# Kernel tuning notes

Hardware: AMD Instinct MI355X
Metric: run time of the kernel (lower is better)

Reference implementation:

```python
import jax, jax.numpy as jnp
import numpy as np

B, N, K = 4, 2048, 20
TD, GD = 64, 128          # trans_dim, graph_dim
OBJ, IMG = 200, 224       # obj_size, img_size
EPS = 1e-5
G = 4                     # GroupNorm groups


def setup_inputs() -> dict:
    key = jax.random.key(0)
    ks = jax.random.split(key, 16)
    nrm = lambda k, shp, s=0.05: jax.random.normal(k, shp, jnp.float32) * s
    inp = {}
    inp["original_pc"] = jax.random.uniform(ks[0], (B, N, 3), jnp.float32)
    inp["pc"] = jax.random.uniform(ks[1], (B, N, 3), jnp.float32)
    # input_trans: Conv1d(3, TD, 1)
    inp["W_in"] = nrm(ks[2], (TD, 3)); inp["b_in"] = jnp.zeros((TD,), jnp.float32)
    # graph_layer: Conv2d(2*TD, GD, 1, bias=False) + GroupNorm(4, GD)
    inp["W_graph"] = nrm(ks[3], (GD, 2 * TD))
    inp["gn_g"] = jnp.ones((GD,), jnp.float32); inp["gn_b"] = jnp.zeros((GD,), jnp.float32)
    # proj_layer: Conv1d(GD, GD, 1)
    inp["W_proj"] = nrm(ks[4], (GD, GD)); inp["b_proj"] = jnp.zeros((GD,), jnp.float32)
    # BasicBlock: conv3x3 + BN (eval) x2
    inp["W1"] = nrm(ks[5], (GD, GD, 3, 3))
    inp["bn1_g"] = jnp.ones((GD,), jnp.float32); inp["bn1_b"] = jnp.zeros((GD,), jnp.float32)
    inp["bn1_m"] = nrm(ks[6], (GD,), 0.1)
    inp["bn1_v"] = jax.random.uniform(ks[7], (GD,), jnp.float32, 0.5, 1.5)
    inp["W2"] = nrm(ks[8], (GD, GD, 3, 3))
    inp["bn2_g"] = jnp.ones((GD,), jnp.float32); inp["bn2_b"] = jnp.zeros((GD,), jnp.float32)
    inp["bn2_m"] = nrm(ks[9], (GD,), 0.1)
    inp["bn2_v"] = jax.random.uniform(ks[10], (GD,), jnp.float32, 0.5, 1.5)
    # img_block tail: Conv2d(GD, GD, 1)
    inp["W_imgc"] = nrm(ks[11], (GD, GD)); inp["b_imgc"] = jnp.zeros((GD,), jnp.float32)
    # img_layer: Conv2d(GD, 3, 1)
    inp["W_img"] = nrm(ks[12], (3, GD)); inp["b_img"] = jnp.zeros((3,), jnp.float32)
    return inp


def reference(original_pc, pc, W_in, b_in, W_graph, gn_g, gn_b, W_proj, b_proj,
              W1, bn1_g, bn1_b, bn1_m, bn1_v, W2, bn2_g, bn2_b, bn2_m, bn2_v,
              W_imgc, b_imgc, W_img, b_img):
    # ---- point feature + knn graph feature ----
    x = jnp.einsum('bnd,cd->bnc', original_pc, W_in) + b_in              # (B,N,TD)
    sq = jnp.sum(original_pc * original_pc, -1)                          # (B,N)
    d2 = sq[:, :, None] + sq[:, None, :] - 2.0 * jnp.einsum('bnd,bmd->bnm', original_pc, original_pc)
    _, idx = jax.lax.top_k(-d2, K)                                       # (B,N,K) knn indices
    nbr = jax.vmap(lambda a, i: a[i])(x, idx)                            # (B,N,K,TD) gather
    xq = x[:, :, None, :]
    feat = jnp.concatenate([nbr - xq, jnp.broadcast_to(xq, nbr.shape)], -1)  # (B,N,K,2TD)
    # edge-conv 1x1 + GroupNorm(4) + LeakyReLU(0.2)
    y = jnp.einsum('bnkc,oc->bnko', feat, W_graph)                       # (B,N,K,GD)
    yg = y.reshape(B, N, K, G, GD // G)
    mu = yg.mean(axis=(1, 2, 4), keepdims=True)
    var = yg.var(axis=(1, 2, 4), keepdims=True)
    y = ((yg - mu) / jnp.sqrt(var + EPS)).reshape(B, N, K, GD) * gn_g + gn_b
    y = jax.nn.leaky_relu(y, 0.2)
    f = y.max(axis=2)                                                    # (B,N,GD) max over k
    f = jnp.einsum('bnc,oc->bno', f, W_proj) + b_proj                    # (B,N,GD)

    # ---- dense-to-grid index math ----
    pmin = pc.min(axis=1); pmax = pc.max(axis=1)                         # (B,3)
    gs = jnp.max((pmax - pmin)[:, :2], axis=-1) / (OBJ - 3)              # (B,)
    ixy = jnp.floor((pc[:, :, :2] - pmin[:, None, :2]) / gs[:, None, None])
    off9 = jnp.array([[-1, -1], [-1, 0], [-1, 1], [0, -1], [0, 0], [0, 1],
                      [1, -1], [1, 0], [1, 1]], jnp.float32)
    dense = (ixy[:, :, None, :] + off9[None, None]).reshape(B, N * 9, 2) + 1.0
    center = jnp.floor((dense.max(axis=1) + dense.min(axis=1)) / 2.0)    # (B,2)
    shift = OBJ / 2 - center - 1.0
    dense = dense + shift[:, None, :]
    lin = (dense[..., 0] * OBJ + dense[..., 1]).astype(jnp.int32)        # (B, N*9)

    fd = jnp.broadcast_to(f[:, :, None, :], (B, N, 9, GD)).reshape(B, N * 9, GD)
    seg = lin + (jnp.arange(B, dtype=jnp.int32) * (OBJ * OBJ))[:, None]
    grid = jax.ops.segment_sum(fd.reshape(-1, GD), seg.reshape(-1), num_segments=B * OBJ * OBJ)
    grid = grid.reshape(B, OBJ, OBJ, GD)
    pad = (IMG - OBJ) // 2
    res = jnp.pad(grid, ((0, 0), (pad, pad), (pad, pad), (0, 0)))
    res = res.transpose(0, 3, 1, 2)                                      # (B,GD,IMG,IMG)

    # ---- BasicBlock (eval BN) + 1x1 convs ----
    conv3 = lambda a, w: jax.lax.conv_general_dilated(a, w, (1, 1), 'SAME',
                         dimension_numbers=('NCHW', 'OIHW', 'NCHW'))
    bn = lambda a, g, b, m, v: (a - m[:, None, None]) / jnp.sqrt(v[:, None, None] + EPS) * g[:, None, None] + b[:, None, None]
    h = jax.nn.relu(bn(conv3(res, W1), bn1_g, bn1_b, bn1_m, bn1_v))
    h = bn(conv3(h, W2), bn2_g, bn2_b, bn2_m, bn2_v)
    h = jax.nn.relu(h + res)
    h = jnp.einsum('bchw,oc->bohw', h, W_imgc) + b_imgc[:, None, None]
    img = jnp.einsum('bchw,oc->bohw', h, W_img) + b_img[:, None, None]
    img = jax.nn.sigmoid(img)
    mean = jnp.array([0.485, 0.456, 0.406], jnp.float32)[None, :, None, None]
    std = jnp.array([0.229, 0.224, 0.225], jnp.float32)[None, :, None, None]
    return (img - mean) / std
```

## Files before the change

### kernel.cpp

```cpp
#include <hip/hip_runtime.h>
#include <stdint.h>

#define NPTS 2048
#define BATCH 4
#define KNN 20
#define EPSV 1e-5f

typedef short bf16x8 __attribute__((ext_vector_type(8)));
typedef float f32x4 __attribute__((ext_vector_type(4)));

__device__ __forceinline__ unsigned short f2bf(float f){
  union { float f; uint32_t u; } x; x.f = f;
  uint32_t u = x.u;
  uint32_t r = (u + 0x7fffu + ((u >> 16) & 1u)) >> 16;
  return (unsigned short)r;
}
__device__ __forceinline__ float bf2f(unsigned short h){
  union { uint32_t u; float f; } x; x.u = ((uint32_t)h) << 16;
  return x.f;
}

__global__ __launch_bounds__(256) void fold_wpk(const float* __restrict__ W, const float* __restrict__ g,
    const float* __restrict__ bb, const float* __restrict__ m, const float* __restrict__ vv,
    unsigned short* __restrict__ w, float* __restrict__ bias){
  int e = blockIdx.x*256 + threadIdx.x;
  if (e < 128){
    float s = g[e] / sqrtf(vv[e] + EPSV);
    bias[e] = bb[e] - m[e]*s;
  }
  if (e < 9*128*128){
    int t = e >> 14;
    int o = (e >> 7) & 127;
    int i = e & 127;
    int kh = t/3, kw = t - 3*kh;
    float s = g[o] / sqrtf(vv[o] + EPSV);
    float wv = W[((o*128 + i)*3 + kh)*3 + kw] * s;
    w[(t*128 + o)*128 + i] = f2bf(wv);
  }
}

__global__ __launch_bounds__(256) void fold_img(const float* __restrict__ Wimgc, const float* __restrict__ bimgc,
    const float* __restrict__ Wimg, const float* __restrict__ bimg,
    float* __restrict__ Wf, float* __restrict__ bf){
  int e = blockIdx.x*256 + threadIdx.x;
  if (e < 384){
    int j = e >> 7, c = e & 127;
    float s = 0.f;
    for (int o = 0; o < 128; ++o) s += Wimg[j*128+o] * Wimgc[o*128+c];
    Wf[e] = s;
  }
  if (e < 3){
    float s = bimg[e];
    for (int o = 0; o < 128; ++o) s += Wimg[e*128+o] * bimgc[o];
    bf[e] = s;
  }
}

__global__ __launch_bounds__(256) void prep_x(const float* __restrict__ opc, const float* __restrict__ Win,
    const float* __restrict__ bin, float* __restrict__ x, double* __restrict__ sq){
  int p = blockIdx.x*256 + threadIdx.x;
  if (p >= BATCH*NPTS) return;
  float a = opc[p*3], b = opc[p*3+1], c = opc[p*3+2];
  double ad = a, bd = b, cd = c;
  sq[p] = (ad*ad + bd*bd) + cd*cd;
  for (int o = 0; o < 64; ++o)
    x[p*64+o] = a*Win[o*3] + b*Win[o*3+1] + c*Win[o*3+2] + bin[o];
}

__global__ __launch_bounds__(256) void prep_uv(const float* __restrict__ x, const float* __restrict__ Wg,
    float* __restrict__ u, float* __restrict__ v){
  int e = blockIdx.x*256 + threadIdx.x;
  if (e >= BATCH*NPTS*128) return;
  int p = e >> 7, o = e & 127;
  const float* xr = x + p*64;
  const float* w = Wg + o*128;
  float su = 0.f, sv = 0.f;
  for (int c = 0; c < 64; ++c){
    float xv = xr[c];
    sv += w[c]*xv;
    su += (w[64+c] - w[c])*xv;
  }
  u[e] = su; v[e] = sv;
}

__device__ __forceinline__ void knn_merge(double va, int ia, double vb, int ib,
                                          double& vo, int& io){
  if (vb < va || (vb == va && ib < ia)){ vo = vb; io = ib; }
  else { vo = va; io = ia; }
}

__device__ __forceinline__ void knn_scan_q(const double* __restrict__ d, int lane, int qt,
                                           double& vq, int& iq){
  double v0 = 1.0e300, v1 = 1.0e300;
  int i0 = -1, i1 = -1;
  int kb = qt*8;
  #pragma unroll
  for (int k2 = 0; k2 < 8; k2 += 2){
    int m0 = lane + (kb + k2)*64;
    int m1 = lane + (kb + k2 + 1)*64;
    double a0 = d[m0];
    double a1 = d[m1];
    if (a0 < v0){ v0 = a0; i0 = m0; }
    if (a1 < v1){ v1 = a1; i1 = m1; }
  }
  knn_merge(v0, i0, v1, i1, vq, iq);
}

__global__ __launch_bounds__(128) void knn_k(const float* __restrict__ pc, const double* __restrict__ sq,
    int* __restrict__ idx){
  __shared__ double dd[2][NPTS];
  int wave = threadIdx.x >> 6, lane = threadIdx.x & 63;
  int q = blockIdx.x*2 + wave;
  int b = q >> 11, n = q & 2047;
  const float* pb = pc + (size_t)b*NPTS*3;
  const double* sqb = sq + b*NPTS;
  double qx = pb[n*3], qy = pb[n*3+1], qz = pb[n*3+2];
  double sn = sqb[n];
  double* d = dd[wave];
  double vq[4]; int iq[4];
  #pragma unroll
  for (int t = 0; t < 4; ++t){ vq[t] = 1.0e300; iq[t] = -1; }
  #pragma unroll
  for (int k = 0; k < 32; ++k){
    int m = lane + k*64;
    double px = pb[m*3], py = pb[m*3+1], pz = pb[m*3+2];
    double dot = (qx*px + qy*py) + qz*pz;
    double val = (sn + sqb[m]) - 2.0*dot;
    d[m] = val;
    const int qt = k >> 3;
    if (val < vq[qt]){ vq[qt] = val; iq[qt] = m; }
  }
  double bv; int bi;
  {
    double m0, m1; int j0, j1;
    knn_merge(vq[0], iq[0], vq[1], iq[1], m0, j0);
    knn_merge(vq[2], iq[2], vq[3], iq[3], m1, j1);
    knn_merge(m0, j0, m1, j1, bv, bi);
  }
  for (int it = 0; it < KNN; ++it){
    double v = bv; int i = bi;
    #pragma unroll
    for (int s = 32; s; s >>= 1){
      double ov = __shfl_xor(v, s);
      int oi = __shfl_xor(i, s);
      if (ov < v || (ov == v && oi < i)){ v = ov; i = oi; }
    }
    if (lane == 0) idx[q*KNN + it] = i;
    if ((i & 63) == lane){
      d[i] = 1.0e300;
      int qt = i >> 9;
      knn_scan_q(d, lane, qt, vq[qt], iq[qt]);
      double m0, m1; int j0, j1;
      knn_merge(vq[0], iq[0], vq[1], iq[1], m0, j0);
      knn_merge(vq[2], iq[2], vq[3], iq[3], m1, j1);
      knn_merge(m0, j0, m1, j1, bv, bi);
    }
  }
}

__global__ __launch_bounds__(256) void stats_k(const float* __restrict__ u, const float* __restrict__ v,
    const int* __restrict__ idx, float* __restrict__ sums){
  int blk = blockIdx.x;
  int b = blk >> 7;
  int n0 = (blk & 127) * 16;
  int tid = threadIdx.x;
  __shared__ int sidx[16*KNN];
  for (int i = tid; i < 16*KNN; i += 256)
    sidx[i] = idx[(b*NPTS + n0 + i/KNN)*KNN + (i % KNN)];
  __syncthreads();
  int c = tid & 127;
  int h = tid >> 7;
  float s = 0.f, ss = 0.f;
  for (int nl = 0; nl < 16; ++nl){
    float uv = u[((b*NPTS + n0 + nl) << 7) + c];
    for (int k = h; k < KNN; k += 2){
      int m = sidx[nl*KNN + k];
      float y = v[((b*NPTS + m) << 7) + c] + uv;
      s += y; ss += y*y;
    }
  }
  for (int msk = 1; msk < 32; msk <<= 1){
    s += __shfl_xor(s, msk);
    ss += __shfl_xor(ss, msk);
  }
  if ((tid & 31) == 0){
    int g = c >> 5;
    atomicAdd(&sums[(b*4 + g)*2 + 0], s);
    atomicAdd(&sums[(b*4 + g)*2 + 1], ss);
  }
}

__global__ __launch_bounds__(256) void fcomp_k(const float* __restrict__ u, const float* __restrict__ v,
    const int* __restrict__ idx, const float* __restrict__ sums,
    const float* __restrict__ gng, const float* __restrict__ gnb,
    const float* __restrict__ Wp, const float* __restrict__ bp, float* __restrict__ f){
  int blk = blockIdx.x;
  int b = blk >> 7;
  int n0 = (blk & 127) * 16;
  int tid = threadIdx.x;
  __shared__ int sidx[16*KNN];
  __shared__ float fpre[16*128];
  __shared__ float smu[4], sinv[4];
  if (tid < 4){
    const float cnt = 2048.0f*20.0f*32.0f;
    float sm = sums[(b*4 + tid)*2 + 0];
    float s2 = sums[(b*4 + tid)*2 + 1];
    float mu = sm/cnt;
    float var = s2/cnt - mu*mu;
    smu[tid] = mu;
    sinv[tid] = 1.0f / sqrtf(var + EPSV);
  }
  for (int i = tid; i < 16*KNN; i += 256)
    sidx[i] = idx[(b*NPTS + n0 + i/KNN)*KNN + (i % KNN)];
  __syncthreads();
  for (int e = tid; e < 2048; e += 256){
    int nl = e >> 7, c = e & 127;
    int g = c >> 5;
    float uv = u[((b*NPTS + n0 + nl) << 7) + c];
    float mu = smu[g], inv = sinv[g], gg = gng[c], gb = gnb[c];
    float best = -3.0e38f;
    for (int k = 0; k < KNN; ++k){
      int m = sidx[nl*KNN + k];
      float y = v[((b*NPTS + m) << 7) + c] + uv;
      float z = (y - mu)*inv*gg + gb;
      z = z >= 0.f ? z : 0.2f*z;
      best = fmaxf(best, z);
    }
    fpre[e] = best;
  }
  __syncthreads();
  for (int e = tid; e < 2048; e += 256){
    int nl = e >> 7, o = e & 127;
    const float* w = Wp + o*128;
    const float* fp = fpre + nl*128;
    float acc = bp[o];
    for (int c2 = 0; c2 < 128; ++c2) acc += fp[c2]*w[c2];
    f[((b*NPTS + n0 + nl) << 7) + o] = acc;
  }
}

__device__ __forceinline__ float blk_red(float val, float* red, int tid, bool ismin){
  for (int s = 32; s; s >>= 1){
    float o = __shfl_xor(val, s);
    val = ismin ? fminf(val, o) : fmaxf(val, o);
  }
  if ((tid & 63) == 0) red[tid >> 6] = val;
  __syncthreads();
  float r = ismin ? fminf(fminf(red[0],red[1]), fminf(red[2],red[3]))
                  : fmaxf(fmaxf(red[0],red[1]), fmaxf(red[2],red[3]));
  __syncthreads();
  return r;
}

__global__ __launch_bounds__(256) void bounds_k(const float* __restrict__ pc, double* __restrict__ bnd){
  __shared__ float red[4];
  int b = blockIdx.x;
  int tid = threadIdx.x;
  const float* p = pc + (size_t)b*NPTS*3;
  float mn0 = 3.0e38f, mn1 = 3.0e38f, mx0 = -3.0e38f, mx1 = -3.0e38f;
  for (int n = tid; n < NPTS; n += 256){
    float a = p[n*3], c = p[n*3+1];
    mn0 = fminf(mn0, a); mx0 = fmaxf(mx0, a);
    mn1 = fminf(mn1, c); mx1 = fmaxf(mx1, c);
  }
  mn0 = blk_red(mn0, red, tid, true);
  mx0 = blk_red(mx0, red, tid, false);
  mn1 = blk_red(mn1, red, tid, true);
  mx1 = blk_red(mx1, red, tid, false);
  double e0 = (double)mx0 - (double)mn0;
  double e1 = (double)mx1 - (double)mn1;
  double gs = (e0 > e1 ? e0 : e1) / 197.0;
  float imn0 = 3.0e38f, imx0 = -3.0e38f, imn1 = 3.0e38f, imx1 = -3.0e38f;
  for (int n = tid; n < NPTS; n += 256){
    float i0 = (float)floor(((double)p[n*3]   - (double)mn0) / gs);
    float i1 = (float)floor(((double)p[n*3+1] - (double)mn1) / gs);
    imn0 = fminf(imn0, i0); imx0 = fmaxf(imx0, i0);
    imn1 = fminf(imn1, i1); imx1 = fmaxf(imx1, i1);
  }
  imn0 = blk_red(imn0, red, tid, true);
  imx0 = blk_red(imx0, red, tid, false);
  imn1 = blk_red(imn1, red, tid, true);
  imx1 = blk_red(imx1, red, tid, false);
  if (tid == 0){
    float c0 = floorf((imx0 + 2.0f + imn0) / 2.0f);
    float c1 = floorf((imx1 + 2.0f + imn1) / 2.0f);
    bnd[b*8+0] = (double)mn0;
    bnd[b*8+1] = (double)mn1;
    bnd[b*8+2] = gs;
    bnd[b*8+3] = (double)(100.0f - c0 - 1.0f);
    bnd[b*8+4] = (double)(100.0f - c1 - 1.0f);
  }
}

__global__ __launch_bounds__(256) void scatter_k(const float* __restrict__ pc, const double* __restrict__ bnd,
    const float* __restrict__ f, float* __restrict__ resf){
  int wave = threadIdx.x >> 6, lane = threadIdx.x & 63;
  int q = blockIdx.x*4 + wave;
  int b = q >> 11;
  const double* bd = bnd + b*8;
  double gs = bd[2];
  double px = pc[(size_t)q*3], py = pc[(size_t)q*3+1];
  int ix0 = (int)floor((px - bd[0]) / gs);
  int iy0 = (int)floor((py - bd[1]) / gs);
  int cx = ix0 + 1 + (int)bd[3];
  int cy = iy0 + 1 + (int)bd[4];
  float f0 = f[(size_t)q*128 + lane];
  float f1 = f[(size_t)q*128 + 64 + lane];
  for (int t = 0; t < 9; ++t){
    int gx = cx + t/3 - 1;
    int gy = cy + t%3 - 1;
    if ((unsigned)gx < 200u && (unsigned)gy < 200u){
      float* cell = resf + (((size_t)b*226 + (gx+13))*226 + (gy+13))*128;
      atomicAdd(cell + lane, f0);
      atomicAdd(cell + 64 + lane, f1);
    }
  }
}

__global__ __launch_bounds__(256) void zbordf_k(float* __restrict__ h1f){
  int i = blockIdx.x*256 + threadIdx.x;
  if (i >= BATCH*900*32) return;
  int chunk = i & 31;
  int pix = i >> 5;
  int b = pix / 900;
  int p = pix - b*900;
  int y, x;
  if (p < 226){ y = 0; x = p; }
  else if (p < 452){ y = 225; x = p - 226; }
  else if (p < 676){ x = 0; y = 1 + (p - 452); }
  else { x = 225; y = 1 + (p - 676); }
  float4 z = {0.f, 0.f, 0.f, 0.f};
  *(float4*)(h1f + (((size_t)b*226 + y)*226 + x)*128 + chunk*4) = z;
}

template<int FUSE_FINAL>
__global__ __launch_bounds__(256) void conv3_k(
    const float* __restrict__ in, const unsigned short* __restrict__ w,
    const float* __restrict__ bias, const float* __restrict__ res,
    float* __restrict__ out, const float* __restrict__ Wf, const float* __restrict__ bff){
  __shared__ __align__(16) char inb[23040];
  __shared__ float facc[8][16][3];
  int tx = blockIdx.x, ty = blockIdx.y, b = blockIdx.z;
  int tid = threadIdx.x;
  int lane = tid & 63, wave = tid >> 6;
  int lo = lane & 15, hi = lane >> 4;
  const int y0 = ty*8, x0 = tx*16;
  const float* ibase = in + (size_t)b*226*226*128;
  if (FUSE_FINAL){
    for (int e = tid; e < 384; e += 256) ((float*)facc)[e] = 0.f;
  }
  f32x4 acc[8][2];
  f32x4 zero = {0.f, 0.f, 0.f, 0.f};
  #pragma unroll
  for (int i = 0; i < 8; ++i){ acc[i][0] = zero; acc[i][1] = zero; }
  int ocb = wave*32;
  int boff0 = (ocb + lo)*128 + hi*8;
  int boff1 = (ocb + 16 + lo)*128 + hi*8;
  for (int ih2 = 0; ih2 < 2; ++ih2){
    __syncthreads();
    for (int ch = tid; ch < 1440; ch += 256){
      int pix = ch >> 3, ci = ch & 7;
      int iy = pix/18, ix = pix - iy*18;
      const float* src = ibase + ((size_t)(y0+iy)*226 + (x0+ix))*128 + ih2*64 + ci*8;
      float4 v0 = *(const float4*)(src);
      float4 v1 = *(const float4*)(src + 4);
      unsigned short h8[8];
      h8[0]=f2bf(v0.x); h8[1]=f2bf(v0.y); h8[2]=f2bf(v0.z); h8[3]=f2bf(v0.w);
      h8[4]=f2bf(v1.x); h8[5]=f2bf(v1.y); h8[6]=f2bf(v1.z); h8[7]=f2bf(v1.w);
      *(bf16x8*)(inb + ((pix*128 + ci*16) ^ ((ix & 7) << 4))) = *(bf16x8*)h8;
    }
    __syncthreads();
    const unsigned short* wb_ = w + ih2*64;
    bf16x8 pb0 = *(const bf16x8*)(wb_ + boff0);
    bf16x8 pb1 = *(const bf16x8*)(wb_ + boff1);
    #pragma unroll 1
    for (int t = 0; t < 9; ++t){
      int dy = t/3, dx = t - 3*dy;
      int ix = lo + dx;
      int swz = (ix & 7) << 4;
      #pragma unroll
      for (int kc = 0; kc < 2; ++kc){
        bf16x8 b0 = pb0, b1 = pb1;
        int nstep = t*2 + kc + 1;
        size_t nb = (size_t)(nstep >> 1)*16384 + (nstep & 1)*32;
        pb0 = *(const bf16x8*)(wb_ + nb + boff0);
        pb1 = *(const bf16x8*)(wb_ + nb + boff1);
        #pragma unroll
        for (int py = 0; py < 8; ++py){
          bf16x8 a = *(const bf16x8*)(inb + ((((py+dy)*18 + ix)*128 + kc*64 + hi*16) ^ swz));
          acc[py][0] = __builtin_amdgcn_mfma_f32_16x16x32_bf16(a, b0, acc[py][0], 0, 0, 0);
          acc[py][1] = __builtin_amdgcn_mfma_f32_16x16x32_bf16(a, b1, acc[py][1], 0, 0, 0);
        }
      }
    }
  }
  if (FUSE_FINAL){
    __syncthreads();
    float wf0[2], wf1[2], wf2[2];
    #pragma unroll
    for (int j = 0; j < 2; ++j){
      int oc = ocb + j*16 + lo;
      wf0[j] = Wf[oc]; wf1[j] = Wf[128+oc]; wf2[j] = Wf[256+oc];
    }
    #pragma unroll
    for (int py = 0; py < 8; ++py){
      int gy = ty*8 + py;
      #pragma unroll
      for (int r = 0; r < 4; ++r){
        int px = hi*4 + r;
        int gx = tx*16 + px;
        float p0 = 0.f, p1 = 0.f, p2 = 0.f;
        #pragma unroll
        for (int j = 0; j < 2; ++j){
          int oc = ocb + j*16 + lo;
          float val = acc[py][j][r] + bias[oc]
                    + res[(((size_t)b*226 + gy+1)*226 + (gx+1))*128 + oc];
          val = fmaxf(val, 0.f);
          p0 += val*wf0[j]; p1 += val*wf1[j]; p2 += val*wf2[j];
        }
        #pragma unroll
        for (int s = 1; s < 16; s <<= 1){
          p0 += __shfl_xor(p0, s);
          p1 += __shfl_xor(p1, s);
          p2 += __shfl_xor(p2, s);
        }
        if (lo == 0){
          atomicAdd(&facc[py][px][0], p0);
          atomicAdd(&facc[py][px][1], p1);
          atomicAdd(&facc[py][px][2], p2);
        }
      }
    }
    __syncthreads();
    const float mean3[3] = {0.485f, 0.456f, 0.406f};
    const float istd3[3] = {1.0f/0.229f, 1.0f/0.224f, 1.0f/0.225f};
    for (int e = tid; e < 384; e += 256){
      int py = e / 48;
      int rem = e - py*48;
      int px = rem / 3;
      int ch = rem - px*3;
      float a = facc[py][px][ch] + bff[ch];
      float s = 1.0f/(1.0f + expf(-a));
      out[(((size_t)(b*3 + ch))*224 + (ty*8+py))*224 + (tx*16+px)] = (s - mean3[ch])*istd3[ch];
    }
  } else {
    #pragma unroll
    for (int py = 0; py < 8; ++py){
      int gy = ty*8 + py;
      #pragma unroll
      for (int j = 0; j < 2; ++j){
        int oc = ocb + j*16 + lo;
        float bs = bias[oc];
        #pragma unroll
        for (int r = 0; r < 4; ++r){
          int px = hi*4 + r;
          int gx = tx*16 + px;
          float val = fmaxf(acc[py][j][r] + bs, 0.f);
          out[(((size_t)b*226 + gy+1)*226 + (gx+1))*128 + oc] = val;
        }
      }
    }
  }
}

extern "C" void kernel_launch(void* const* d_in, const int* in_sizes, int n_in,
                              void* d_out, int out_size, void* d_ws, size_t ws_size,
                              hipStream_t stream){
  const float* opc   = (const float*)d_in[0];
  const float* pc    = (const float*)d_in[1];
  const float* Win   = (const float*)d_in[2];
  const float* bin   = (const float*)d_in[3];
  const float* Wg    = (const float*)d_in[4];
  const float* gng   = (const float*)d_in[5];
  const float* gnb   = (const float*)d_in[6];
  const float* Wp    = (const float*)d_in[7];
  const float* bp    = (const float*)d_in[8];
  const float* W1    = (const float*)d_in[9];
  const float* g1    = (const float*)d_in[10];
  const float* b1    = (const float*)d_in[11];
  const float* m1    = (const float*)d_in[12];
  const float* v1    = (const float*)d_in[13];
  const float* W2    = (const float*)d_in[14];
  const float* g2    = (const float*)d_in[15];
  const float* b2    = (const float*)d_in[16];
  const float* m2    = (const float*)d_in[17];
  const float* v2    = (const float*)d_in[18];
  const float* Wimgc = (const float*)d_in[19];
  const float* bimgc = (const float*)d_in[20];
  const float* Wimg  = (const float*)d_in[21];
  const float* bimg  = (const float*)d_in[22];

  char* ws = (char*)d_ws;
  size_t off = 0;
  auto alloc = [&](size_t bytes)->char*{
    char* p = ws + off;
    off += (bytes + 255) & ~(size_t)255;
    return p;
  };
  float* x      = (float*)alloc((size_t)BATCH*NPTS*64*4);
  double* sq    = (double*)alloc((size_t)BATCH*NPTS*8);
  int*   idx    = (int*)  alloc((size_t)BATCH*NPTS*KNN*4);
  float* u      = (float*)alloc((size_t)BATCH*NPTS*128*4);
  float* v      = (float*)alloc((size_t)BATCH*NPTS*128*4);
  float* f      = (float*)alloc((size_t)BATCH*NPTS*128*4);
  float* sums   = (float*)alloc(256);
  double* bnd   = (double*)alloc(256);
  float* bias1  = (float*)alloc(512);
  float* bias2  = (float*)alloc(512);
  float* Wf     = (float*)alloc(2048);
  float* bff    = (float*)alloc(256);
  unsigned short* w1f = (unsigned short*)alloc((size_t)10*16384*2);
  unsigned short* w2f = (unsigned short*)alloc((size_t)10*16384*2);
  float* resf = (float*)alloc((size_t)BATCH*226*226*128*4);
  float* h1f  = (float*)alloc((size_t)BATCH*226*226*128*4);
  float* out = (float*)d_out;

  hipMemsetAsync(sums, 0, 256, stream);
  hipMemsetAsync(resf, 0, (size_t)BATCH*226*226*128*4, stream);

  fold_wpk<<<576, 256, 0, stream>>>(W1, g1, b1, m1, v1, w1f, bias1);
  fold_wpk<<<576, 256, 0, stream>>>(W2, g2, b2, m2, v2, w2f, bias2);
  fold_img<<<2, 256, 0, stream>>>(Wimgc, bimgc, Wimg, bimg, Wf, bff);
  zbordf_k<<<450, 256, 0, stream>>>(h1f);
  prep_x<<<32, 256, 0, stream>>>(opc, Win, bin, x, sq);
  prep_uv<<<4096, 256, 0, stream>>>(x, Wg, u, v);
  knn_k<<<4096, 128, 0, stream>>>(opc, sq, idx);
  stats_k<<<512, 256, 0, stream>>>(u, v, idx, sums);
  fcomp_k<<<512, 256, 0, stream>>>(u, v, idx, sums, gng, gnb, Wp, bp, f);
  bounds_k<<<4, 256, 0, stream>>>(pc, bnd);
  scatter_k<<<2048, 256, 0, stream>>>(pc, bnd, f, resf);
  conv3_k<0><<<dim3(14,28,4), 256, 0, stream>>>(resf, w1f, bias1, nullptr, h1f, nullptr, nullptr);
  conv3_k<1><<<dim3(14,28,4), 256, 0, stream>>>(h1f, w2f, bias2, resf, out, Wf, bff);
}
```

Before: 579.9 us.

## Store conv intermediate as bf16 and precompute max/min neighbor value in stats pass

The first 3x3 conv now writes its ReLU output as bf16 through a shared-memory staging buffer with coalesced 16-byte stores. The second conv reads that bf16 buffer directly instead of loading fp32 and converting. This halves the intermediate traffic and drops a conversion step. Separately, stats_k records the per-channel max or min over the K neighbors (chosen by the sign of the GroupNorm gamma), so fcomp_k no longer re-gathers all neighbor features; this relies on GroupNorm plus LeakyReLU being monotonic per channel.

```diff
diff --git a/kernel.cpp b/kernel.cpp
--- a/kernel.cpp
+++ b/kernel.cpp
@@ -7,6 +7,7 @@
 #define EPSV 1e-5f
 
 typedef short bf16x8 __attribute__((ext_vector_type(8)));
+typedef unsigned short u16x8 __attribute__((ext_vector_type(8)));
 typedef float f32x4 __attribute__((ext_vector_type(4)));
 
 __device__ __forceinline__ unsigned short f2bf(float f){
@@ -159,7 +160,8 @@
 }
 
 __global__ __launch_bounds__(256) void stats_k(const float* __restrict__ u, const float* __restrict__ v,
-    const int* __restrict__ idx, float* __restrict__ sums){
+    const int* __restrict__ idx, const float* __restrict__ gng,
+    float* __restrict__ sums, float* __restrict__ ysel){
   int blk = blockIdx.x;
   int b = blk >> 7;
   int n0 = (blk & 127) * 16;
@@ -169,15 +171,20 @@
     sidx[i] = idx[(b*NPTS + n0 + i/KNN)*KNN + (i % KNN)];
   __syncthreads();
   int c = tid & 127;
-  int h = tid >> 7;
+  int nh = tid >> 7;
+  float gg = gng[c];
   float s = 0.f, ss = 0.f;
-  for (int nl = 0; nl < 16; ++nl){
+  for (int nl = nh*8; nl < nh*8 + 8; ++nl){
     float uv = u[((b*NPTS + n0 + nl) << 7) + c];
-    for (int k = h; k < KNN; k += 2){
+    float best = -3.0e38f, worst = 3.0e38f;
+    for (int k = 0; k < KNN; ++k){
       int m = sidx[nl*KNN + k];
       float y = v[((b*NPTS + m) << 7) + c] + uv;
       s += y; ss += y*y;
-    }
+      best = fmaxf(best, y);
+      worst = fminf(worst, y);
+    }
+    ysel[((b*NPTS + n0 + nl) << 7) + c] = (gg >= 0.f) ? best : worst;
   }
   for (int msk = 1; msk < 32; msk <<= 1){
     s += __shfl_xor(s, msk);
@@ -190,15 +197,14 @@
   }
 }
 
-__global__ __launch_bounds__(256) void fcomp_k(const float* __restrict__ u, const float* __restrict__ v,
-    const int* __restrict__ idx, const float* __restrict__ sums,
+__global__ __launch_bounds__(256) void fcomp_k(const float* __restrict__ ysel,
+    const float* __restrict__ sums,
     const float* __restrict__ gng, const float* __restrict__ gnb,
     const float* __restrict__ Wp, const float* __restrict__ bp, float* __restrict__ f){
   int blk = blockIdx.x;
   int b = blk >> 7;
   int n0 = (blk & 127) * 16;
   int tid = threadIdx.x;
-  __shared__ int sidx[16*KNN];
   __shared__ float fpre[16*128];
   __shared__ float smu[4], sinv[4];
   if (tid < 4){
@@ -210,23 +216,14 @@
     smu[tid] = mu;
     sinv[tid] = 1.0f / sqrtf(var + EPSV);
   }
-  for (int i = tid; i < 16*KNN; i += 256)
-    sidx[i] = idx[(b*NPTS + n0 + i/KNN)*KNN + (i % KNN)];
   __syncthreads();
   for (int e = tid; e < 2048; e += 256){
     int nl = e >> 7, c = e & 127;
     int g = c >> 5;
-    float uv = u[((b*NPTS + n0 + nl) << 7) + c];
-    float mu = smu[g], inv = sinv[g], gg = gng[c], gb = gnb[c];
-    float best = -3.0e38f;
-    for (int k = 0; k < KNN; ++k){
-      int m = sidx[nl*KNN + k];
-      float y = v[((b*NPTS + m) << 7) + c] + uv;
-      float z = (y - mu)*inv*gg + gb;
-      z = z >= 0.f ? z : 0.2f*z;
-      best = fmaxf(best, z);
-    }
-    fpre[e] = best;
+    float y = ysel[((b*NPTS + n0 + nl) << 7) + c];
+    float z = (y - smu[g])*sinv[g]*gng[c] + gnb[c];
+    z = z >= 0.f ? z : 0.2f*z;
+    fpre[e] = z;
   }
   __syncthreads();
   for (int e = tid; e < 2048; e += 256){
@@ -317,11 +314,11 @@
   }
 }
 
-__global__ __launch_bounds__(256) void zbordf_k(float* __restrict__ h1f){
+__global__ __launch_bounds__(256) void zbordb_k(unsigned short* __restrict__ h1b){
   int i = blockIdx.x*256 + threadIdx.x;
-  if (i >= BATCH*900*32) return;
-  int chunk = i & 31;
-  int pix = i >> 5;
+  if (i >= BATCH*900*16) return;
+  int chunk = i & 15;
+  int pix = i >> 4;
   int b = pix / 900;
   int p = pix - b*900;
   int y, x;
@@ -329,23 +326,25 @@
   else if (p < 452){ y = 225; x = p - 226; }
   else if (p < 676){ x = 0; y = 1 + (p - 452); }
   else { x = 225; y = 1 + (p - 676); }
-  float4 z = {0.f, 0.f, 0.f, 0.f};
-  *(float4*)(h1f + (((size_t)b*226 + y)*226 + x)*128 + chunk*4) = z;
-}
-
-template<int FUSE_FINAL>
+  u16x8 z = {0,0,0,0,0,0,0,0};
+  *(u16x8*)(h1b + (((size_t)b*226 + y)*226 + x)*128 + chunk*8) = z;
+}
+
+template<int IN_BF16, int FUSE_FINAL>
 __global__ __launch_bounds__(256) void conv3_k(
-    const float* __restrict__ in, const unsigned short* __restrict__ w,
-    const float* __restrict__ bias, const float* __restrict__ res,
-    float* __restrict__ out, const float* __restrict__ Wf, const float* __restrict__ bff){
-  __shared__ __align__(16) char inb[23040];
+    const float* __restrict__ inf, const unsigned short* __restrict__ inh,
+    const unsigned short* __restrict__ w, const float* __restrict__ bias,
+    const float* __restrict__ res, float* __restrict__ out, unsigned short* __restrict__ outh,
+    const float* __restrict__ Wf, const float* __restrict__ bff){
+  __shared__ __align__(16) char inb[32768];
   __shared__ float facc[8][16][3];
   int tx = blockIdx.x, ty = blockIdx.y, b = blockIdx.z;
   int tid = threadIdx.x;
   int lane = tid & 63, wave = tid >> 6;
   int lo = lane & 15, hi = lane >> 4;
   const int y0 = ty*8, x0 = tx*16;
-  const float* ibase = in + (size_t)b*226*226*128;
+  const float* ibase = IN_BF16 ? nullptr : (inf + (size_t)b*226*226*128);
+  const unsigned short* ihb = IN_BF16 ? (inh + (size_t)b*226*226*128) : nullptr;
   if (FUSE_FINAL){
     for (int e = tid; e < 384; e += 256) ((float*)facc)[e] = 0.f;
   }
@@ -361,13 +360,19 @@
     for (int ch = tid; ch < 1440; ch += 256){
       int pix = ch >> 3, ci = ch & 7;
       int iy = pix/18, ix = pix - iy*18;
-      const float* src = ibase + ((size_t)(y0+iy)*226 + (x0+ix))*128 + ih2*64 + ci*8;
-      float4 v0 = *(const float4*)(src);
-      float4 v1 = *(const float4*)(src + 4);
-      unsigned short h8[8];
-      h8[0]=f2bf(v0.x); h8[1]=f2bf(v0.y); h8[2]=f2bf(v0.z); h8[3]=f2bf(v0.w);
-      h8[4]=f2bf(v1.x); h8[5]=f2bf(v1.y); h8[6]=f2bf(v1.z); h8[7]=f2bf(v1.w);
-      *(bf16x8*)(inb + ((pix*128 + ci*16) ^ ((ix & 7) << 4))) = *(bf16x8*)h8;
+      size_t poff = (size_t)(y0+iy)*226 + (x0+ix);
+      int dst = (pix*128 + ci*16) ^ ((ix & 7) << 4);
+      if (IN_BF16){
+        *(u16x8*)(inb + dst) = *(const u16x8*)(ihb + poff*128 + ih2*64 + ci*8);
+      } else {
+        const float* src = ibase + poff*128 + ih2*64 + ci*8;
+        float4 v0 = *(const float4*)(src);
+        float4 v1 = *(const float4*)(src + 4);
+        unsigned short h8[8];
+        h8[0]=f2bf(v0.x); h8[1]=f2bf(v0.y); h8[2]=f2bf(v0.z); h8[3]=f2bf(v0.w);
+        h8[4]=f2bf(v1.x); h8[5]=f2bf(v1.y); h8[6]=f2bf(v1.z); h8[7]=f2bf(v1.w);
+        *(bf16x8*)(inb + dst) = *(bf16x8*)h8;
+      }
     }
     __syncthreads();
     const unsigned short* wb_ = w + ih2*64;
@@ -444,21 +449,28 @@
       out[(((size_t)(b*3 + ch))*224 + (ty*8+py))*224 + (tx*16+px)] = (s - mean3[ch])*istd3[ch];
     }
   } else {
+    __syncthreads();
     #pragma unroll
     for (int py = 0; py < 8; ++py){
-      int gy = ty*8 + py;
       #pragma unroll
       for (int j = 0; j < 2; ++j){
         int oc = ocb + j*16 + lo;
         float bs = bias[oc];
         #pragma unroll
         for (int r = 0; r < 4; ++r){
-          int px = hi*4 + r;
-          int gx = tx*16 + px;
+          int pix = py*16 + hi*4 + r;
           float val = fmaxf(acc[py][j][r] + bs, 0.f);
-          out[(((size_t)b*226 + gy+1)*226 + (gx+1))*128 + oc] = val;
+          *(unsigned short*)(inb + pix*256 + oc*2) = f2bf(val);
         }
       }
+    }
+    __syncthreads();
+    unsigned short* ob = outh + (size_t)b*226*226*128;
+    for (int e = tid; e < 2048; e += 256){
+      int pix = e >> 4, cg = e & 15;
+      int py = pix >> 4, px = pix & 15;
+      u16x8 val = *(u16x8*)(inb + pix*256 + cg*16);
+      *(u16x8*)(ob + (((size_t)(y0+py+1))*226 + (x0+px+1))*128 + cg*8) = val;
     }
   }
 }
@@ -502,6 +514,7 @@
   int*   idx    = (int*)  alloc((size_t)BATCH*NPTS*KNN*4);
   float* u      = (float*)alloc((size_t)BATCH*NPTS*128*4);
   float* v      = (float*)alloc((size_t)BATCH*NPTS*128*4);
+  float* ysel   = (float*)alloc((size_t)BATCH*NPTS*128*4);
   float* f      = (float*)alloc((size_t)BATCH*NPTS*128*4);
   float* sums   = (float*)alloc(256);
   double* bnd   = (double*)alloc(256);
@@ -511,8 +524,8 @@
   float* bff    = (float*)alloc(256);
   unsigned short* w1f = (unsigned short*)alloc((size_t)10*16384*2);
   unsigned short* w2f = (unsigned short*)alloc((size_t)10*16384*2);
-  float* resf = (float*)alloc((size_t)BATCH*226*226*128*4);
-  float* h1f  = (float*)alloc((size_t)BATCH*226*226*128*4);
+  float* resf         = (float*)alloc((size_t)BATCH*226*226*128*4);
+  unsigned short* h1b = (unsigned short*)alloc((size_t)BATCH*226*226*128*2);
   float* out = (float*)d_out;
 
   hipMemsetAsync(sums, 0, 256, stream);
@@ -521,14 +534,14 @@
   fold_wpk<<<576, 256, 0, stream>>>(W1, g1, b1, m1, v1, w1f, bias1);
   fold_wpk<<<576, 256, 0, stream>>>(W2, g2, b2, m2, v2, w2f, bias2);
   fold_img<<<2, 256, 0, stream>>>(Wimgc, bimgc, Wimg, bimg, Wf, bff);
-  zbordf_k<<<450, 256, 0, stream>>>(h1f);
+  zbordb_k<<<225, 256, 0, stream>>>(h1b);
   prep_x<<<32, 256, 0, stream>>>(opc, Win, bin, x, sq);
   prep_uv<<<4096, 256, 0, stream>>>(x, Wg, u, v);
   knn_k<<<4096, 128, 0, stream>>>(opc, sq, idx);
-  stats_k<<<512, 256, 0, stream>>>(u, v, idx, sums);
-  fcomp_k<<<512, 256, 0, stream>>>(u, v, idx, sums, gng, gnb, Wp, bp, f);
+  stats_k<<<512, 256, 0, stream>>>(u, v, idx, gng, sums, ysel);
+  fcomp_k<<<512, 256, 0, stream>>>(ysel, sums, gng, gnb, Wp, bp, f);
   bounds_k<<<4, 256, 0, stream>>>(pc, bnd);
   scatter_k<<<2048, 256, 0, stream>>>(pc, bnd, f, resf);
-  conv3_k<0><<<dim3(14,28,4), 256, 0, stream>>>(resf, w1f, bias1, nullptr, h1f, nullptr, nullptr);
-  conv3_k<1><<<dim3(14,28,4), 256, 0, stream>>>(h1f, w2f, bias2, resf, out, Wf, bff);
-}
+  conv3_k<0,0><<<dim3(14,28,4), 256, 0, stream>>>(resf, nullptr, w1f, bias1, nullptr, nullptr, h1b, nullptr, nullptr);
+  conv3_k<1,1><<<dim3(14,28,4), 256, 0, stream>>>(nullptr, h1b, w2f, bias2, resf, out, nullptr, Wf, bff);
+}
```

New measurement: 537.3 us. 1.08x faster.
